# Kernel tuning notes

Hardware: AMD Instinct MI355X
Metric: run time of the kernel (lower is better)

## Reference

```python
import jax, jax.numpy as jnp
import numpy as np

B, S, D_MODEL, D_ATTN = 4, 2048, 1024, 1024
NEG_INF = jnp.float32(-jnp.inf)


def setup_inputs() -> dict:
    key = jax.random.key(0)
    ks = jax.random.split(key, 6)
    scale = 1.0 / np.sqrt(D_MODEL)
    return {
        "x": jax.random.normal(ks[0], (B, S, D_MODEL), dtype=jnp.float32),
        "mask": jnp.ones((B, S), dtype=jnp.float32),
        "Wq": jax.random.normal(ks[1], (D_ATTN, D_MODEL), dtype=jnp.float32) * scale,
        "Wk": jax.random.normal(ks[2], (D_ATTN, D_MODEL), dtype=jnp.float32) * scale,
        "Wv": jax.random.normal(ks[3], (D_ATTN, D_MODEL), dtype=jnp.float32) * scale,
        "Wo": jax.random.normal(ks[4], (D_MODEL, D_ATTN), dtype=jnp.float32) * scale,
        "bo": jnp.zeros((D_MODEL,), dtype=jnp.float32),
    }


def reference(x, mask, Wq, Wk, Wv, Wo, bo):
    # x: [B,S,Dm]; torch Linear weight is [out,in], so y = x @ W.T
    q = jnp.einsum("bsd,ad->bsa", x, Wq)  # [B,S,Da]
    k = jnp.einsum("bsd,ad->bsa", x, Wk)
    v = jnp.einsum("bsd,ad->bsa", x, Wv)  # NOTE: v from x (original quirk)
    logits = jnp.einsum("bqa,bka->bqk", q, k)  # [B,S,S]
    # causal mask (cross_attention=True path): keep lower triangle incl. diag
    causal = jnp.tril(jnp.ones((S, S), dtype=bool))
    logits = jnp.where(causal[None], logits, NEG_INF)
    # padding mask: outer product of per-token mask
    square_mask = mask[:, :, None] * mask[:, None, :]  # [B,S,S]
    logits = jnp.where(square_mask == 1, logits, NEG_INF)
    # scale by sqrt(d_model) AFTER masking (as in original)
    attn = jax.nn.softmax(logits / jnp.sqrt(jnp.float32(D_MODEL)), axis=-1)
    attn_out = jnp.einsum("bqk,bka->bqa", attn, v)  # [B,S,Da]
    return jnp.einsum("bsa,da->bsd", attn_out, Wo) + bo
```

## Files before the change

kernel.cpp:

```cpp
#include <hip/hip_runtime.h>
#include <hip/hip_bf16.h>
#include <cstdio>

typedef __bf16 bf16x8 __attribute__((ext_vector_type(8)));
typedef float f32x4 __attribute__((ext_vector_type(4)));

#define BM 128
#define BN 128
#define BK 64

__device__ __forceinline__ unsigned short f2bf(float f) {
  union { float f; unsigned u; } v; v.f = f;
  unsigned u = v.u;
  return (unsigned short)((u + 0x7FFFu + ((u >> 16) & 1u)) >> 16);
}

__device__ __forceinline__ float bf2f(unsigned short s) {
  union { unsigned u; float f; } v; v.u = ((unsigned)s) << 16;
  return v.f;
}

#define GLOAD16(gsrc, ldst) \
  __builtin_amdgcn_global_load_lds((const __attribute__((address_space(1))) void*)(gsrc), \
                                   (__attribute__((address_space(3))) void*)(ldst), 16, 0, 0)

template<int EPI>
__global__ __launch_bounds__(256, 2)
void gemm_bt(const unsigned short* __restrict__ A, const unsigned short* __restrict__ B,
             void* __restrict__ Cv, void* __restrict__ Cv2, const float* __restrict__ bias,
             int K, int ldA, int ldB, int ldC,
             long aBat, long bBat, long cBat,
             int causalSkip, int causalKlim, float scale, int revM)
{
  const int gx = gridDim.x;
  const int nwg = gx * gridDim.y;
  const int flat = blockIdx.y * gx + blockIdx.x;
  const int qch = nwg >> 3, rch = nwg & 7;
  const int xcd = flat & 7, idx = flat >> 3;
  const int swz = (xcd < rch ? xcd * (qch + 1) : rch * (qch + 1) + (xcd - rch) * qch) + idx;
  const int bx = swz % gx;
  int by = swz / gx;
  if (revM) by = gridDim.y - 1 - by;

  const int m0 = by * BM;
  const int n0 = bx * BN;
  if (causalSkip && n0 > m0) return;
  const int bz = blockIdx.z;

  const unsigned short* Ab = A + (long)bz * aBat + (long)m0 * ldA;
  const unsigned short* Bb = B + (long)bz * bBat + (long)n0 * ldB;

  __shared__ short lds[2][2][BM * BK];

  const int tid = threadIdx.x;
  const int lane = tid & 63;
  const int wave = tid >> 6;
  const int wr = wave >> 1, wc = wave & 1;

  const int Keff = causalKlim ? min(K, m0 + BM) : K;
  const int nk = Keff / BK;

  const int srow = tid >> 3;
  const int sch = tid & 7;

  const f32x4 fzero = {0.f, 0.f, 0.f, 0.f};
  f32x4 acc[4][4];
#pragma unroll
  for (int i = 0; i < 4; i++)
#pragma unroll
    for (int j = 0; j < 4; j++) acc[i][j] = fzero;

  int aOff[4][2], bOff[4][2];
#pragma unroll
  for (int i = 0; i < 4; i++) {
#pragma unroll
    for (int s = 0; s < 2; s++) {
      int ra = wr * 64 + i * 16 + (lane & 15);
      aOff[i][s] = ra * BK + (((s * 4 + (lane >> 4)) ^ (ra & 7)) * 8);
      int rb = wc * 64 + i * 16 + (lane & 15);
      bOff[i][s] = rb * BK + (((s * 4 + (lane >> 4)) ^ (rb & 7)) * 8);
    }
  }

  auto stage = [&](int buf, int kt) {
    const unsigned short* Ak = Ab + kt * BK;
    const unsigned short* Bk = Bb + kt * BK;
#pragma unroll
    for (int r = 0; r < 4; r++) {
      int row = r * 32 + srow;
      int sc = sch ^ (row & 7);
      GLOAD16(Ak + (long)row * ldA + sc * 8, &lds[buf][0][(r * 32 + wave * 8) * BK]);
    }
#pragma unroll
    for (int r = 0; r < 4; r++) {
      int row = r * 32 + srow;
      int sc = sch ^ (row & 7);
      GLOAD16(Bk + (long)row * ldB + sc * 8, &lds[buf][1][(r * 32 + wave * 8) * BK]);
    }
  };

  stage(0, 0);
  stage(1, 1);
  asm volatile("s_waitcnt vmcnt(8)" ::: "memory");
  __builtin_amdgcn_sched_barrier(0);
  __builtin_amdgcn_s_barrier();

  int cur = 0;
  for (int kt = 0; kt < nk; kt++) {
    const short* La = lds[cur][0];
    const short* Lb = lds[cur][1];
    bf16x8 av[2][4], bv[2][4];
#pragma unroll
    for (int s = 0; s < 2; s++) {
#pragma unroll
      for (int i = 0; i < 4; i++) {
        av[s][i] = *reinterpret_cast<const bf16x8*>(La + aOff[i][s]);
        bv[s][i] = *reinterpret_cast<const bf16x8*>(Lb + bOff[i][s]);
      }
    }
    asm volatile("s_waitcnt lgkmcnt(0)" ::: "memory");
    __builtin_amdgcn_sched_barrier(0);
    __builtin_amdgcn_s_barrier();
    __builtin_amdgcn_sched_barrier(0);

    if (kt + 2 < nk) {
      stage(cur, kt + 2);
      asm volatile("s_waitcnt vmcnt(8)" ::: "memory");
    } else if (kt + 1 < nk) {
      asm volatile("s_waitcnt vmcnt(0)" ::: "memory");
    }
    if (kt + 1 < nk) {
      __builtin_amdgcn_s_barrier();
      __builtin_amdgcn_sched_barrier(0);
    }

    __builtin_amdgcn_s_setprio(1);
#pragma unroll
    for (int s = 0; s < 2; s++)
#pragma unroll
      for (int i = 0; i < 4; i++)
#pragma unroll
        for (int j = 0; j < 4; j++)
          acc[i][j] = __builtin_amdgcn_mfma_f32_16x16x32_bf16(av[s][i], bv[s][j], acc[i][j], 0, 0, 0);
    __builtin_amdgcn_s_setprio(0);
    __builtin_amdgcn_sched_barrier(0);
    cur ^= 1;
  }

  const int rb4 = (lane >> 4) * 4;
  const int cl = lane & 15;
#pragma unroll
  for (int i = 0; i < 4; i++) {
#pragma unroll
    for (int j = 0; j < 4; j++) {
      const int gm = m0 + wr * 64 + i * 16 + rb4;
      const int gn = n0 + wc * 64 + j * 16 + cl;
      if (EPI == 0) {
        unsigned short* C = (unsigned short*)Cv + (long)bz * cBat;
#pragma unroll
        for (int r = 0; r < 4; r++)
          C[(long)(gm + r) * ldC + gn] = f2bf(acc[i][j][r] * scale);
      } else if (EPI == 2) {
        float* C = (float*)Cv;
        const float bb = bias[gn];
#pragma unroll
        for (int r = 0; r < 4; r++)
          C[(long)(gm + r) * ldC + gn] = acc[i][j][r] + bb;
      } else if (EPI == 4) {
        if (gn < 2048) {
          unsigned short* C = (unsigned short*)Cv;
#pragma unroll
          for (int r = 0; r < 4; r++)
            C[(long)(gm + r) * ldC + gn] = f2bf(acc[i][j][r]);
        } else {
          const int d = gn - 2048;
          const int b = gm >> 11;
          const int sIdx = gm & 2047;
          unsigned short* C = (unsigned short*)Cv2 + (long)b * (2048L * 1024)
                              + (long)d * 2048 + sIdx;
          ushort4 pk;
          pk.x = f2bf(acc[i][j][0]);
          pk.y = f2bf(acc[i][j][1]);
          pk.z = f2bf(acc[i][j][2]);
          pk.w = f2bf(acc[i][j][3]);
          *reinterpret_cast<ushort4*>(C) = pk;
        }
      }
    }
  }
}

__global__ __launch_bounds__(256)
void softmax_rows(const unsigned short* __restrict__ Sb, const float* __restrict__ maskv,
                  unsigned short* __restrict__ P, int Sdim)
{
  const int q = blockIdx.x;
  const int b = blockIdx.y;
  const int kmax = (q & ~127) + 128;
  const unsigned short* row = Sb + ((long)b * Sdim + q) * Sdim;
  unsigned short* prow = P + ((long)b * Sdim + q) * Sdim;
  const float* mrow = maskv + (long)b * Sdim;
  const int tid = threadIdx.x;
  const float mq = mrow[q];
  const int k0 = tid * 8;
  const bool live = (k0 < kmax);

  float v[8];
  if (live) {
    uint4 raw = *reinterpret_cast<const uint4*>(row + k0);
    const unsigned short* us = reinterpret_cast<const unsigned short*>(&raw);
    float4 ma = *reinterpret_cast<const float4*>(mrow + k0);
    float4 mb = *reinterpret_cast<const float4*>(mrow + k0 + 4);
    float mv[8] = {ma.x, ma.y, ma.z, ma.w, mb.x, mb.y, mb.z, mb.w};
#pragma unroll
    for (int u = 0; u < 8; u++) {
      const int k = k0 + u;
      const bool ok = (k <= q) && (mq * mv[u] == 1.0f);
      v[u] = ok ? bf2f(us[u]) : -INFINITY;
    }
  } else {
#pragma unroll
    for (int u = 0; u < 8; u++) v[u] = -INFINITY;
  }

  float mx = -INFINITY;
#pragma unroll
  for (int u = 0; u < 8; u++) mx = fmaxf(mx, v[u]);
#pragma unroll
  for (int o = 32; o; o >>= 1) mx = fmaxf(mx, __shfl_xor(mx, o));
  __shared__ float redm[4], reds[4];
  if ((tid & 63) == 0) redm[tid >> 6] = mx;
  __syncthreads();
  mx = fmaxf(fmaxf(redm[0], redm[1]), fmaxf(redm[2], redm[3]));

  float p[8];
  float sm = 0.f;
#pragma unroll
  for (int u = 0; u < 8; u++) {
    p[u] = (v[u] > -INFINITY) ? __expf(v[u] - mx) : 0.f;
    sm += p[u];
  }
#pragma unroll
  for (int o = 32; o; o >>= 1) sm += __shfl_xor(sm, o);
  if ((tid & 63) == 0) reds[tid >> 6] = sm;
  __syncthreads();
  sm = reds[0] + reds[1] + reds[2] + reds[3];
  const float inv = 1.0f / sm;

  if (live) {
    union { unsigned short us[8]; uint4 u4; } pk;
#pragma unroll
    for (int u = 0; u < 8; u++) pk.us[u] = f2bf(p[u] * inv);
    *reinterpret_cast<uint4*>(prow + k0) = pk.u4;
  }
}

__global__ __launch_bounds__(256)
void cast_f32_bf16(const float* __restrict__ in, unsigned short* __restrict__ out, int n)
{
  const int i = (blockIdx.x * 256 + threadIdx.x) * 8;
  if (i >= n) return;
  float4 a = *reinterpret_cast<const float4*>(in + i);
  float4 b = *reinterpret_cast<const float4*>(in + i + 4);
  union { unsigned short us[8]; uint4 u4; } pk;
  pk.us[0] = f2bf(a.x); pk.us[1] = f2bf(a.y); pk.us[2] = f2bf(a.z); pk.us[3] = f2bf(a.w);
  pk.us[4] = f2bf(b.x); pk.us[5] = f2bf(b.y); pk.us[6] = f2bf(b.z); pk.us[7] = f2bf(b.w);
  *reinterpret_cast<uint4*>(out + i) = pk.u4;
}

__global__ __launch_bounds__(256)
void cast_weights(const float* __restrict__ w0, const float* __restrict__ w1,
                  const float* __restrict__ w2, const float* __restrict__ w3,
                  unsigned short* __restrict__ dqkv, unsigned short* __restrict__ dout)
{
  const int z = blockIdx.z;
  const float* src = (z == 0) ? w0 : (z == 1) ? w1 : (z == 2) ? w2 : w3;
  unsigned short* dst = (z < 3) ? (dqkv + (long)z * 1024 * 1024) : dout;
  const int i = (blockIdx.x * 256 + threadIdx.x) * 8;
  float4 a = *reinterpret_cast<const float4*>(src + i);
  float4 b = *reinterpret_cast<const float4*>(src + i + 4);
  union { unsigned short us[8]; uint4 u4; } pk;
  pk.us[0] = f2bf(a.x); pk.us[1] = f2bf(a.y); pk.us[2] = f2bf(a.z); pk.us[3] = f2bf(a.w);
  pk.us[4] = f2bf(b.x); pk.us[5] = f2bf(b.y); pk.us[6] = f2bf(b.z); pk.us[7] = f2bf(b.w);
  *reinterpret_cast<uint4*>(dst + i) = pk.u4;
}

extern "C" void kernel_launch(void* const* d_in, const int* in_sizes, int n_in,
                              void* d_out, int out_size, void* d_ws, size_t ws_size,
                              hipStream_t stream)
{
  const int B = 4, S = 2048, D = 1024;
  const float* x  = (const float*)d_in[0];
  const float* mk = (const float*)d_in[1];
  const float* Wq = (const float*)d_in[2];
  const float* Wk = (const float*)d_in[3];
  const float* Wv = (const float*)d_in[4];
  const float* Wo = (const float*)d_in[5];
  const float* bo = (const float*)d_in[6];
  float* out = (float*)d_out;

  char* ws = (char*)d_ws;
  const long MB = 1024L * 1024L;
  unsigned short* Xbf  = (unsigned short*)(ws + 0);
  unsigned short* QKb  = (unsigned short*)(ws + 16 * MB);
  unsigned short* Vt   = (unsigned short*)(ws + 48 * MB);
  unsigned short* Wqkv = (unsigned short*)(ws + 64 * MB);
  unsigned short* Wob  = (unsigned short*)(ws + 70 * MB);
  unsigned short* Sbuf = (unsigned short*)(ws + 72 * MB);
  unsigned short* P    = QKb;
  unsigned short* O    = Xbf;

  if (ws_size < (size_t)(104 * MB)) {
    fprintf(stderr, "kernel_launch: ws too small (%zu bytes, need 104MB)\n", ws_size);
    return;
  }

  cast_f32_bf16<<<dim3((B * S * D) / 8 / 256), 256, 0, stream>>>(x, Xbf, B * S * D);
  cast_weights<<<dim3((D * D) / 8 / 256, 1, 4), 256, 0, stream>>>(Wq, Wk, Wv, Wo, Wqkv, Wob);

  const dim3 blk(256);
  dim3 gQKV(3072 / BN, 8192 / BM, 1);
  gemm_bt<4><<<gQKV, blk, 0, stream>>>(Xbf, Wqkv, QKb, Vt, nullptr,
                                       1024, 1024, 1024, 2048,
                                       0, 0, 0, 0, 0, 1.0f, 0);
  dim3 gS(2048 / BN, 2048 / BM, 4);
  gemm_bt<0><<<gS, blk, 0, stream>>>(QKb, QKb + 1024, Sbuf, nullptr, nullptr,
                                     1024, 2048, 2048, 2048,
                                     (long)S * 2048, (long)S * 2048, (long)S * S,
                                     1, 0, 0.03125f, 0);
  softmax_rows<<<dim3(2048, 4), blk, 0, stream>>>(Sbuf, mk, P, 2048);
  dim3 gO(1024 / BN, 2048 / BM, 4);
  gemm_bt<0><<<gO, blk, 0, stream>>>(P, Vt, O, nullptr, nullptr,
                                     2048, 2048, 2048, 1024,
                                     (long)S * S, (long)D * S, (long)S * D,
                                     0, 1, 1.0f, 1);
  dim3 gF(1024 / BN, 8192 / BM, 1);
  gemm_bt<2><<<gF, blk, 0, stream>>>(O, Wob, out, nullptr, bo,
                                     1024, 1024, 1024, 1024,
                                     0, 0, 0, 0, 0, 1.0f, 0);
}
```

Baseline: 180.7 us.

## Widen GEMM tile to 128x256 with 8 waves and interleaved quarter-step pipeline

GEMM blocks grow to 512 threads (8 waves in a 2x4 layout) covering 128x256 output tiles. Each k-step is split into four MFMA quarters interleaved with LDS fragment loads and staggered global-to-LDS staging of the next A and B tiles. The causal skip test is adjusted to the wider N tile. The two cast kernels are merged into a single launch. The aim is more operand reuse per LDS byte and better overlap of memory with MFMA, at the cost of one block per CU, fewer blocks for the smaller GEMMs, and more wasted work in causal tiles.

```diff
diff --git a/kernel.cpp b/kernel.cpp
--- a/kernel.cpp
+++ b/kernel.cpp
@@ -6,7 +6,7 @@
 typedef float f32x4 __attribute__((ext_vector_type(4)));
 
 #define BM 128
-#define BN 128
+#define BN 256
 #define BK 64
 
 __device__ __forceinline__ unsigned short f2bf(float f) {
@@ -25,7 +25,7 @@
                                    (__attribute__((address_space(3))) void*)(ldst), 16, 0, 0)
 
 template<int EPI>
-__global__ __launch_bounds__(256, 2)
+__global__ __launch_bounds__(512, 1)
 void gemm_bt(const unsigned short* __restrict__ A, const unsigned short* __restrict__ B,
              void* __restrict__ Cv, void* __restrict__ Cv2, const float* __restrict__ bias,
              int K, int ldA, int ldB, int ldC,
@@ -44,18 +44,19 @@
 
   const int m0 = by * BM;
   const int n0 = bx * BN;
-  if (causalSkip && n0 > m0) return;
+  if (causalSkip && n0 > m0 + (BM - 1)) return;
   const int bz = blockIdx.z;
 
   const unsigned short* Ab = A + (long)bz * aBat + (long)m0 * ldA;
   const unsigned short* Bb = B + (long)bz * bBat + (long)n0 * ldB;
 
-  __shared__ short lds[2][2][BM * BK];
+  __shared__ short ldsA[2][BM * BK];
+  __shared__ short ldsB[2][BN * BK];
 
   const int tid = threadIdx.x;
   const int lane = tid & 63;
   const int wave = tid >> 6;
-  const int wr = wave >> 1, wc = wave & 1;
+  const int wr = wave >> 2, wc = wave & 3;
 
   const int Keff = causalKlim ? min(K, m0 + BM) : K;
   const int nk = Keff / BK;
@@ -72,79 +73,133 @@
 
   int aOff[4][2], bOff[4][2];
 #pragma unroll
-  for (int i = 0; i < 4; i++) {
-#pragma unroll
-    for (int s = 0; s < 2; s++) {
-      int ra = wr * 64 + i * 16 + (lane & 15);
-      aOff[i][s] = ra * BK + (((s * 4 + (lane >> 4)) ^ (ra & 7)) * 8);
-      int rb = wc * 64 + i * 16 + (lane & 15);
-      bOff[i][s] = rb * BK + (((s * 4 + (lane >> 4)) ^ (rb & 7)) * 8);
-    }
-  }
-
-  auto stage = [&](int buf, int kt) {
+  for (int f = 0; f < 4; f++) {
+#pragma unroll
+    for (int k = 0; k < 2; k++) {
+      int ra = wr * 64 + f * 16 + (lane & 15);
+      aOff[f][k] = ra * BK + (((k * 4 + (lane >> 4)) ^ (ra & 7)) * 8);
+      int rb = wc * 64 + f * 16 + (lane & 15);
+      bOff[f][k] = rb * BK + (((k * 4 + (lane >> 4)) ^ (rb & 7)) * 8);
+    }
+  }
+
+  auto stageA = [&](int buf, int kt) {
     const unsigned short* Ak = Ab + kt * BK;
+#pragma unroll
+    for (int L = 0; L < 2; L++) {
+      int row = L * 64 + srow;
+      int sc = sch ^ (row & 7);
+      GLOAD16(Ak + (long)row * ldA + sc * 8, &ldsA[buf][row * BK + sch * 8]);
+    }
+  };
+  auto stageB = [&](int buf, int kt, int h) {
     const unsigned short* Bk = Bb + kt * BK;
 #pragma unroll
-    for (int r = 0; r < 4; r++) {
-      int row = r * 32 + srow;
+    for (int L = 0; L < 2; L++) {
+      int row = h * 128 + L * 64 + srow;
       int sc = sch ^ (row & 7);
-      GLOAD16(Ak + (long)row * ldA + sc * 8, &lds[buf][0][(r * 32 + wave * 8) * BK]);
-    }
-#pragma unroll
-    for (int r = 0; r < 4; r++) {
-      int row = r * 32 + srow;
-      int sc = sch ^ (row & 7);
-      GLOAD16(Bk + (long)row * ldB + sc * 8, &lds[buf][1][(r * 32 + wave * 8) * BK]);
+      GLOAD16(Bk + (long)row * ldB + sc * 8, &ldsB[buf][row * BK + sch * 8]);
     }
   };
 
-  stage(0, 0);
-  stage(1, 1);
-  asm volatile("s_waitcnt vmcnt(8)" ::: "memory");
+  stageA(0, 0); stageB(0, 0, 0); stageB(0, 0, 1);
+  if (nk > 1) {
+    stageB(1, 1, 0); stageB(1, 1, 1);
+    asm volatile("s_waitcnt vmcnt(4)" ::: "memory");
+  } else {
+    asm volatile("s_waitcnt vmcnt(0)" ::: "memory");
+  }
   __builtin_amdgcn_sched_barrier(0);
   __builtin_amdgcn_s_barrier();
-
-  int cur = 0;
+  __builtin_amdgcn_sched_barrier(0);
+
   for (int kt = 0; kt < nk; kt++) {
-    const short* La = lds[cur][0];
-    const short* Lb = lds[cur][1];
-    bf16x8 av[2][4], bv[2][4];
-#pragma unroll
-    for (int s = 0; s < 2; s++) {
-#pragma unroll
-      for (int i = 0; i < 4; i++) {
-        av[s][i] = *reinterpret_cast<const bf16x8*>(La + aOff[i][s]);
-        bv[s][i] = *reinterpret_cast<const bf16x8*>(Lb + bOff[i][s]);
-      }
-    }
+    const int cur = kt & 1;
+    const short* La = ldsA[cur];
+    const short* Lb = ldsB[cur];
+    bf16x8 a01[2][2], a23[2][2], b01[2][2], b23[2][2];
+
+#pragma unroll
+    for (int m = 0; m < 2; m++)
+#pragma unroll
+      for (int k = 0; k < 2; k++) a01[m][k] = *reinterpret_cast<const bf16x8*>(La + aOff[m][k]);
+#pragma unroll
+    for (int n = 0; n < 2; n++)
+#pragma unroll
+      for (int k = 0; k < 2; k++) b01[n][k] = *reinterpret_cast<const bf16x8*>(Lb + bOff[n][k]);
+    if (kt + 1 < nk) stageA(cur ^ 1, kt + 1);
+    __builtin_amdgcn_s_barrier();
     asm volatile("s_waitcnt lgkmcnt(0)" ::: "memory");
     __builtin_amdgcn_sched_barrier(0);
-    __builtin_amdgcn_s_barrier();
+    __builtin_amdgcn_s_setprio(1);
+#pragma unroll
+    for (int m = 0; m < 2; m++)
+#pragma unroll
+      for (int n = 0; n < 2; n++)
+#pragma unroll
+        for (int k = 0; k < 2; k++)
+          acc[m][n] = __builtin_amdgcn_mfma_f32_16x16x32_bf16(a01[m][k], b01[n][k], acc[m][n], 0, 0, 0);
+    __builtin_amdgcn_s_setprio(0);
+    __builtin_amdgcn_s_barrier();
+
+#pragma unroll
+    for (int n = 0; n < 2; n++)
+#pragma unroll
+      for (int k = 0; k < 2; k++) b23[n][k] = *reinterpret_cast<const bf16x8*>(Lb + bOff[n + 2][k]);
+    __builtin_amdgcn_s_barrier();
+    asm volatile("s_waitcnt lgkmcnt(0)" ::: "memory");
     __builtin_amdgcn_sched_barrier(0);
-
-    if (kt + 2 < nk) {
-      stage(cur, kt + 2);
-      asm volatile("s_waitcnt vmcnt(8)" ::: "memory");
-    } else if (kt + 1 < nk) {
-      asm volatile("s_waitcnt vmcnt(0)" ::: "memory");
-    }
+    __builtin_amdgcn_s_setprio(1);
+#pragma unroll
+    for (int m = 0; m < 2; m++)
+#pragma unroll
+      for (int n = 0; n < 2; n++)
+#pragma unroll
+        for (int k = 0; k < 2; k++)
+          acc[m][n + 2] = __builtin_amdgcn_mfma_f32_16x16x32_bf16(a01[m][k], b23[n][k], acc[m][n + 2], 0, 0, 0);
+    __builtin_amdgcn_s_setprio(0);
+    __builtin_amdgcn_s_barrier();
+
+#pragma unroll
+    for (int m = 0; m < 2; m++)
+#pragma unroll
+      for (int k = 0; k < 2; k++) a23[m][k] = *reinterpret_cast<const bf16x8*>(La + aOff[m + 2][k]);
+    if (kt + 2 < nk) stageB(cur, kt + 2, 0);
+    __builtin_amdgcn_s_barrier();
+    asm volatile("s_waitcnt lgkmcnt(0)" ::: "memory");
+    __builtin_amdgcn_sched_barrier(0);
+    __builtin_amdgcn_s_setprio(1);
+#pragma unroll
+    for (int m = 0; m < 2; m++)
+#pragma unroll
+      for (int n = 0; n < 2; n++)
+#pragma unroll
+        for (int k = 0; k < 2; k++)
+          acc[m + 2][n] = __builtin_amdgcn_mfma_f32_16x16x32_bf16(a23[m][k], b01[n][k], acc[m + 2][n], 0, 0, 0);
+    __builtin_amdgcn_s_setprio(0);
+    __builtin_amdgcn_s_barrier();
+
+    if (kt + 2 < nk) stageB(cur, kt + 2, 1);
+    __builtin_amdgcn_s_barrier();
+    __builtin_amdgcn_s_setprio(1);
+#pragma unroll
+    for (int m = 0; m < 2; m++)
+#pragma unroll
+      for (int n = 0; n < 2; n++)
+#pragma unroll
+        for (int k = 0; k < 2; k++)
+          acc[m + 2][n + 2] = __builtin_amdgcn_mfma_f32_16x16x32_bf16(a23[m][k], b23[n][k], acc[m + 2][n + 2], 0, 0, 0);
+    __builtin_amdgcn_s_setprio(0);
     if (kt + 1 < nk) {
+      if (kt + 2 < nk) {
+        asm volatile("s_waitcnt vmcnt(4)" ::: "memory");
+      } else {
+        asm volatile("s_waitcnt vmcnt(0)" ::: "memory");
+      }
+      __builtin_amdgcn_sched_barrier(0);
       __builtin_amdgcn_s_barrier();
       __builtin_amdgcn_sched_barrier(0);
     }
-
-    __builtin_amdgcn_s_setprio(1);
-#pragma unroll
-    for (int s = 0; s < 2; s++)
-#pragma unroll
-      for (int i = 0; i < 4; i++)
-#pragma unroll
-        for (int j = 0; j < 4; j++)
-          acc[i][j] = __builtin_amdgcn_mfma_f32_16x16x32_bf16(av[s][i], bv[s][j], acc[i][j], 0, 0, 0);
-    __builtin_amdgcn_s_setprio(0);
-    __builtin_amdgcn_sched_barrier(0);
-    cur ^= 1;
   }
 
   const int rb4 = (lane >> 4) * 4;
@@ -256,27 +311,25 @@
 }
 
 __global__ __launch_bounds__(256)
-void cast_f32_bf16(const float* __restrict__ in, unsigned short* __restrict__ out, int n)
+void cast_all(const float* __restrict__ x, const float* __restrict__ w0,
+              const float* __restrict__ w1, const float* __restrict__ w2,
+              const float* __restrict__ w3,
+              unsigned short* __restrict__ xb, unsigned short* __restrict__ dqkv,
+              unsigned short* __restrict__ dout)
 {
-  const int i = (blockIdx.x * 256 + threadIdx.x) * 8;
-  if (i >= n) return;
-  float4 a = *reinterpret_cast<const float4*>(in + i);
-  float4 b = *reinterpret_cast<const float4*>(in + i + 4);
-  union { unsigned short us[8]; uint4 u4; } pk;
-  pk.us[0] = f2bf(a.x); pk.us[1] = f2bf(a.y); pk.us[2] = f2bf(a.z); pk.us[3] = f2bf(a.w);
-  pk.us[4] = f2bf(b.x); pk.us[5] = f2bf(b.y); pk.us[6] = f2bf(b.z); pk.us[7] = f2bf(b.w);
-  *reinterpret_cast<uint4*>(out + i) = pk.u4;
-}
-
-__global__ __launch_bounds__(256)
-void cast_weights(const float* __restrict__ w0, const float* __restrict__ w1,
-                  const float* __restrict__ w2, const float* __restrict__ w3,
-                  unsigned short* __restrict__ dqkv, unsigned short* __restrict__ dout)
-{
-  const int z = blockIdx.z;
-  const float* src = (z == 0) ? w0 : (z == 1) ? w1 : (z == 2) ? w2 : w3;
-  unsigned short* dst = (z < 3) ? (dqkv + (long)z * 1024 * 1024) : dout;
-  const int i = (blockIdx.x * 256 + threadIdx.x) * 8;
+  const int blk = blockIdx.x;
+  const float* src;
+  unsigned short* dst;
+  int i;
+  if (blk < 4096) {
+    src = x; dst = xb; i = (blk * 256 + threadIdx.x) * 8;
+  } else {
+    const int w = (blk - 4096) >> 9;
+    const int off = (blk - 4096) & 511;
+    src = (w == 0) ? w0 : (w == 1) ? w1 : (w == 2) ? w2 : w3;
+    dst = (w < 3) ? (dqkv + (long)w * 1024 * 1024) : dout;
+    i = (off * 256 + threadIdx.x) * 8;
+  }
   float4 a = *reinterpret_cast<const float4*>(src + i);
   float4 b = *reinterpret_cast<const float4*>(src + i + 4);
   union { unsigned short us[8]; uint4 u4; } pk;
@@ -315,10 +368,9 @@
     return;
   }
 
-  cast_f32_bf16<<<dim3((B * S * D) / 8 / 256), 256, 0, stream>>>(x, Xbf, B * S * D);
-  cast_weights<<<dim3((D * D) / 8 / 256, 1, 4), 256, 0, stream>>>(Wq, Wk, Wv, Wo, Wqkv, Wob);
-
-  const dim3 blk(256);
+  cast_all<<<dim3(4096 + 2048), 256, 0, stream>>>(x, Wq, Wk, Wv, Wo, Xbf, Wqkv, Wob);
+
+  const dim3 blk(512);
   dim3 gQKV(3072 / BN, 8192 / BM, 1);
   gemm_bt<4><<<gQKV, blk, 0, stream>>>(Xbf, Wqkv, QKb, Vt, nullptr,
                                        1024, 1024, 1024, 2048,
@@ -328,7 +380,7 @@
                                      1024, 2048, 2048, 2048,
                                      (long)S * 2048, (long)S * 2048, (long)S * S,
                                      1, 0, 0.03125f, 0);
-  softmax_rows<<<dim3(2048, 4), blk, 0, stream>>>(Sbuf, mk, P, 2048);
+  softmax_rows<<<dim3(2048, 4), dim3(256), 0, stream>>>(Sbuf, mk, P, 2048);
   dim3 gO(1024 / BN, 2048 / BM, 4);
   gemm_bt<0><<<gO, blk, 0, stream>>>(P, Vt, O, nullptr, nullptr,
                                      2048, 2048, 2048, 1024,
```

New measurement: 214.9 us. 18.9% more time.

## Add 256x256-tile 8-wave GEMM for QKV projection and merge cast kernels

Applied to the files above, without the earlier changes.

Replaces the 128x128 QKV projection GEMM with a dedicated 256x256-tile kernel using 512 threads, double-buffered LDS staged by direct global-to-LDS loads, and a staggered A/B prefetch interleaved with four MFMA phases. The larger tile raises arithmetic intensity and cuts global traffic for the biggest GEMM. In exchange it uses one block per CU and a 384-block grid, which may leave CUs underfilled. The x and weight cast kernels are also merged into one launch to save launch overhead.

```diff
diff --git a/kernel.cpp b/kernel.cpp
--- a/kernel.cpp
+++ b/kernel.cpp
@@ -24,10 +24,203 @@
   __builtin_amdgcn_global_load_lds((const __attribute__((address_space(1))) void*)(gsrc), \
                                    (__attribute__((address_space(3))) void*)(ldst), 16, 0, 0)
 
+__global__ __launch_bounds__(512, 1)
+void gemm256_qkv(const unsigned short* __restrict__ A, const unsigned short* __restrict__ B,
+                 unsigned short* __restrict__ QK, unsigned short* __restrict__ Vt,
+                 int K, int ldA, int ldB)
+{
+  const int gx = gridDim.x;
+  const int nwg = gx * gridDim.y;
+  const int flat = blockIdx.y * gx + blockIdx.x;
+  const int qch = nwg >> 3, rch = nwg & 7;
+  const int xcd = flat & 7, idx = flat >> 3;
+  const int swz = (xcd < rch ? xcd * (qch + 1) : rch * (qch + 1) + (xcd - rch) * qch) + idx;
+  const int bx = swz % gx;
+  const int by = swz / gx;
+  const int m0 = by * 256, n0 = bx * 256;
+
+  const unsigned short* Ab = A + (long)m0 * ldA;
+  const unsigned short* Bb = B + (long)n0 * ldB;
+
+  __shared__ short ldsA[2][2][128 * 64];
+  __shared__ short ldsB[2][2][128 * 64];
+
+  const int tid = threadIdx.x;
+  const int lane = tid & 63;
+  const int wave = tid >> 6;
+  const int wr = wave >> 2, wc = wave & 3;
+
+  const int nk = K / 64;
+
+  const int srow = tid >> 3;
+  const int sch = tid & 7;
+  const int ssc = sch ^ (srow & 7);
+
+  f32x4 acc[8][4];
+  const f32x4 fzero = {0.f, 0.f, 0.f, 0.f};
+#pragma unroll
+  for (int i = 0; i < 8; i++)
+#pragma unroll
+    for (int j = 0; j < 4; j++) acc[i][j] = fzero;
+
+  const int rowbase = (lane & 15) * 64;
+  const int x0 = (((lane >> 4) + 0) ^ (lane & 7)) * 8;
+  const int x1 = (((lane >> 4) + 4) ^ (lane & 7)) * 8;
+
+  auto stageA = [&](int buf, int kt, int h) {
+    const unsigned short* src = Ab + (long)(h * 128) * ldA + kt * 64;
+#pragma unroll
+    for (int L = 0; L < 2; L++) {
+      int row = L * 64 + srow;
+      GLOAD16(src + (long)row * ldA + ssc * 8, &ldsA[buf][h][row * 64 + sch * 8]);
+    }
+  };
+  auto stageB = [&](int buf, int kt, int h) {
+    const unsigned short* src = Bb + (long)(h * 128) * ldB + kt * 64;
+#pragma unroll
+    for (int L = 0; L < 2; L++) {
+      int row = L * 64 + srow;
+      GLOAD16(src + (long)row * ldB + ssc * 8, &ldsB[buf][h][row * 64 + sch * 8]);
+    }
+  };
+
+  stageA(0, 0, 0); stageA(0, 0, 1); stageB(0, 0, 0); stageB(0, 0, 1);
+  if (nk > 1) {
+    stageB(1, 1, 0); stageB(1, 1, 1);
+    asm volatile("s_waitcnt vmcnt(4)" ::: "memory");
+  } else {
+    asm volatile("s_waitcnt vmcnt(0)" ::: "memory");
+  }
+  __builtin_amdgcn_sched_barrier(0);
+  __builtin_amdgcn_s_barrier();
+  __builtin_amdgcn_sched_barrier(0);
+
+  for (int kt = 0; kt < nk; kt++) {
+    const int c = kt & 1;
+    const short* pa = &ldsA[c][wr][rowbase];
+    const short* pb = &ldsB[c][wc >> 1][(wc & 1) * 4096 + rowbase];
+    bf16x8 b[4][2];
+    bf16x8 a[2][2];
+
+#pragma unroll
+    for (int f = 0; f < 2; f++) {
+      a[f][0] = *reinterpret_cast<const bf16x8*>(pa + f * 1024 + x0);
+      a[f][1] = *reinterpret_cast<const bf16x8*>(pa + f * 1024 + x1);
+    }
+#pragma unroll
+    for (int f = 0; f < 4; f++) {
+      b[f][0] = *reinterpret_cast<const bf16x8*>(pb + f * 1024 + x0);
+      b[f][1] = *reinterpret_cast<const bf16x8*>(pb + f * 1024 + x1);
+    }
+    if (kt + 1 < nk) { stageA(c ^ 1, kt + 1, 0); stageA(c ^ 1, kt + 1, 1); }
+    asm volatile("s_waitcnt lgkmcnt(0)" ::: "memory");
+    __builtin_amdgcn_sched_barrier(0);
+    __builtin_amdgcn_s_setprio(1);
+#pragma unroll
+    for (int f = 0; f < 2; f++)
+#pragma unroll
+      for (int j = 0; j < 4; j++)
+#pragma unroll
+        for (int k = 0; k < 2; k++)
+          acc[f][j] = __builtin_amdgcn_mfma_f32_16x16x32_bf16(a[f][k], b[j][k], acc[f][j], 0, 0, 0);
+    __builtin_amdgcn_s_setprio(0);
+    __builtin_amdgcn_s_barrier();
+
+#pragma unroll
+    for (int f = 0; f < 2; f++) {
+      a[f][0] = *reinterpret_cast<const bf16x8*>(pa + (f + 2) * 1024 + x0);
+      a[f][1] = *reinterpret_cast<const bf16x8*>(pa + (f + 2) * 1024 + x1);
+    }
+    if (kt + 2 < nk) stageB(c, kt + 2, 0);
+    asm volatile("s_waitcnt lgkmcnt(0)" ::: "memory");
+    __builtin_amdgcn_sched_barrier(0);
+    __builtin_amdgcn_s_setprio(1);
+#pragma unroll
+    for (int f = 0; f < 2; f++)
+#pragma unroll
+      for (int j = 0; j < 4; j++)
+#pragma unroll
+        for (int k = 0; k < 2; k++)
+          acc[f + 2][j] = __builtin_amdgcn_mfma_f32_16x16x32_bf16(a[f][k], b[j][k], acc[f + 2][j], 0, 0, 0);
+    __builtin_amdgcn_s_setprio(0);
+    __builtin_amdgcn_s_barrier();
+
+#pragma unroll
+    for (int f = 0; f < 2; f++) {
+      a[f][0] = *reinterpret_cast<const bf16x8*>(pa + (f + 4) * 1024 + x0);
+      a[f][1] = *reinterpret_cast<const bf16x8*>(pa + (f + 4) * 1024 + x1);
+    }
+    if (kt + 2 < nk) stageB(c, kt + 2, 1);
+    asm volatile("s_waitcnt lgkmcnt(0)" ::: "memory");
+    __builtin_amdgcn_sched_barrier(0);
+    __builtin_amdgcn_s_setprio(1);
+#pragma unroll
+    for (int f = 0; f < 2; f++)
+#pragma unroll
+      for (int j = 0; j < 4; j++)
+#pragma unroll
+        for (int k = 0; k < 2; k++)
+          acc[f + 4][j] = __builtin_amdgcn_mfma_f32_16x16x32_bf16(a[f][k], b[j][k], acc[f + 4][j], 0, 0, 0);
+    __builtin_amdgcn_s_setprio(0);
+    __builtin_amdgcn_s_barrier();
+
+#pragma unroll
+    for (int f = 0; f < 2; f++) {
+      a[f][0] = *reinterpret_cast<const bf16x8*>(pa + (f + 6) * 1024 + x0);
+      a[f][1] = *reinterpret_cast<const bf16x8*>(pa + (f + 6) * 1024 + x1);
+    }
+    asm volatile("s_waitcnt lgkmcnt(0)" ::: "memory");
+    __builtin_amdgcn_sched_barrier(0);
+    __builtin_amdgcn_s_setprio(1);
+#pragma unroll
+    for (int f = 0; f < 2; f++)
+#pragma unroll
+      for (int j = 0; j < 4; j++)
+#pragma unroll
+        for (int k = 0; k < 2; k++)
+          acc[f + 6][j] = __builtin_amdgcn_mfma_f32_16x16x32_bf16(a[f][k], b[j][k], acc[f + 6][j], 0, 0, 0);
+    __builtin_amdgcn_s_setprio(0);
+    if (kt + 1 < nk) {
+      if (kt + 2 < nk) asm volatile("s_waitcnt vmcnt(4)" ::: "memory");
+      else             asm volatile("s_waitcnt vmcnt(0)" ::: "memory");
+      __builtin_amdgcn_sched_barrier(0);
+    }
+    __builtin_amdgcn_s_barrier();
+    __builtin_amdgcn_sched_barrier(0);
+  }
+
+  const int rb4 = (lane >> 4) * 4;
+  const int cl = lane & 15;
+#pragma unroll
+  for (int fi = 0; fi < 8; fi++) {
+#pragma unroll
+    for (int fj = 0; fj < 4; fj++) {
+      const int gm = m0 + wr * 128 + fi * 16 + rb4;
+      const int gn = n0 + wc * 64 + fj * 16 + cl;
+      if (gn < 2048) {
+#pragma unroll
+        for (int r = 0; r < 4; r++)
+          QK[(long)(gm + r) * 2048 + gn] = f2bf(acc[fi][fj][r]);
+      } else {
+        const int d = gn - 2048;
+        const int bb = gm >> 11;
+        const int sIdx = gm & 2047;
+        unsigned short* C = Vt + (long)bb * (2048L * 1024) + (long)d * 2048 + sIdx;
+        ushort4 pk;
+        pk.x = f2bf(acc[fi][fj][0]);
+        pk.y = f2bf(acc[fi][fj][1]);
+        pk.z = f2bf(acc[fi][fj][2]);
+        pk.w = f2bf(acc[fi][fj][3]);
+        *reinterpret_cast<ushort4*>(C) = pk;
+      }
+    }
+  }
+}
+
 template<int EPI>
 __global__ __launch_bounds__(256, 2)
 void gemm_bt(const unsigned short* __restrict__ A, const unsigned short* __restrict__ B,
-             void* __restrict__ Cv, void* __restrict__ Cv2, const float* __restrict__ bias,
+             void* __restrict__ Cv, const float* __restrict__ bias,
              int K, int ldA, int ldB, int ldC,
              long aBat, long bBat, long cBat,
              int causalSkip, int causalKlim, float scale, int revM)
@@ -160,31 +353,12 @@
 #pragma unroll
         for (int r = 0; r < 4; r++)
           C[(long)(gm + r) * ldC + gn] = f2bf(acc[i][j][r] * scale);
-      } else if (EPI == 2) {
+      } else {
         float* C = (float*)Cv;
         const float bb = bias[gn];
 #pragma unroll
         for (int r = 0; r < 4; r++)
           C[(long)(gm + r) * ldC + gn] = acc[i][j][r] + bb;
-      } else if (EPI == 4) {
-        if (gn < 2048) {
-          unsigned short* C = (unsigned short*)Cv;
-#pragma unroll
-          for (int r = 0; r < 4; r++)
-            C[(long)(gm + r) * ldC + gn] = f2bf(acc[i][j][r]);
-        } else {
-          const int d = gn - 2048;
-          const int b = gm >> 11;
-          const int sIdx = gm & 2047;
-          unsigned short* C = (unsigned short*)Cv2 + (long)b * (2048L * 1024)
-                              + (long)d * 2048 + sIdx;
-          ushort4 pk;
-          pk.x = f2bf(acc[i][j][0]);
-          pk.y = f2bf(acc[i][j][1]);
-          pk.z = f2bf(acc[i][j][2]);
-          pk.w = f2bf(acc[i][j][3]);
-          *reinterpret_cast<ushort4*>(C) = pk;
-        }
       }
     }
   }
@@ -256,27 +430,25 @@
 }
 
 __global__ __launch_bounds__(256)
-void cast_f32_bf16(const float* __restrict__ in, unsigned short* __restrict__ out, int n)
+void cast_all(const float* __restrict__ x, const float* __restrict__ w0,
+              const float* __restrict__ w1, const float* __restrict__ w2,
+              const float* __restrict__ w3,
+              unsigned short* __restrict__ xb, unsigned short* __restrict__ dqkv,
+              unsigned short* __restrict__ dout)
 {
-  const int i = (blockIdx.x * 256 + threadIdx.x) * 8;
-  if (i >= n) return;
-  float4 a = *reinterpret_cast<const float4*>(in + i);
-  float4 b = *reinterpret_cast<const float4*>(in + i + 4);
-  union { unsigned short us[8]; uint4 u4; } pk;
-  pk.us[0] = f2bf(a.x); pk.us[1] = f2bf(a.y); pk.us[2] = f2bf(a.z); pk.us[3] = f2bf(a.w);
-  pk.us[4] = f2bf(b.x); pk.us[5] = f2bf(b.y); pk.us[6] = f2bf(b.z); pk.us[7] = f2bf(b.w);
-  *reinterpret_cast<uint4*>(out + i) = pk.u4;
-}
-
-__global__ __launch_bounds__(256)
-void cast_weights(const float* __restrict__ w0, const float* __restrict__ w1,
-                  const float* __restrict__ w2, const float* __restrict__ w3,
-                  unsigned short* __restrict__ dqkv, unsigned short* __restrict__ dout)
-{
-  const int z = blockIdx.z;
-  const float* src = (z == 0) ? w0 : (z == 1) ? w1 : (z == 2) ? w2 : w3;
-  unsigned short* dst = (z < 3) ? (dqkv + (long)z * 1024 * 1024) : dout;
-  const int i = (blockIdx.x * 256 + threadIdx.x) * 8;
+  const int blk = blockIdx.x;
+  const float* src;
+  unsigned short* dst;
+  int i;
+  if (blk < 4096) {
+    src = x; dst = xb; i = (blk * 256 + threadIdx.x) * 8;
+  } else {
+    const int w = (blk - 4096) >> 9;
+    const int off = (blk - 4096) & 511;
+    src = (w == 0) ? w0 : (w == 1) ? w1 : (w == 2) ? w2 : w3;
+    dst = (w < 3) ? (dqkv + (long)w * 1024 * 1024) : dout;
+    i = (off * 256 + threadIdx.x) * 8;
+  }
   float4 a = *reinterpret_cast<const float4*>(src + i);
   float4 b = *reinterpret_cast<const float4*>(src + i + 4);
   union { unsigned short us[8]; uint4 u4; } pk;
@@ -315,27 +487,24 @@
     return;
   }
 
-  cast_f32_bf16<<<dim3((B * S * D) / 8 / 256), 256, 0, stream>>>(x, Xbf, B * S * D);
-  cast_weights<<<dim3((D * D) / 8 / 256, 1, 4), 256, 0, stream>>>(Wq, Wk, Wv, Wo, Wqkv, Wob);
+  cast_all<<<dim3(4096 + 2048), 256, 0, stream>>>(x, Wq, Wk, Wv, Wo, Xbf, Wqkv, Wob);
+
+  gemm256_qkv<<<dim3(12, 32), dim3(512), 0, stream>>>(Xbf, Wqkv, QKb, Vt, 1024, 1024, 1024);
 
   const dim3 blk(256);
-  dim3 gQKV(3072 / BN, 8192 / BM, 1);
-  gemm_bt<4><<<gQKV, blk, 0, stream>>>(Xbf, Wqkv, QKb, Vt, nullptr,
-                                       1024, 1024, 1024, 2048,
-                                       0, 0, 0, 0, 0, 1.0f, 0);
   dim3 gS(2048 / BN, 2048 / BM, 4);
-  gemm_bt<0><<<gS, blk, 0, stream>>>(QKb, QKb + 1024, Sbuf, nullptr, nullptr,
+  gemm_bt<0><<<gS, blk, 0, stream>>>(QKb, QKb + 1024, Sbuf, nullptr,
                                      1024, 2048, 2048, 2048,
                                      (long)S * 2048, (long)S * 2048, (long)S * S,
                                      1, 0, 0.03125f, 0);
   softmax_rows<<<dim3(2048, 4), blk, 0, stream>>>(Sbuf, mk, P, 2048);
   dim3 gO(1024 / BN, 2048 / BM, 4);
-  gemm_bt<0><<<gO, blk, 0, stream>>>(P, Vt, O, nullptr, nullptr,
+  gemm_bt<0><<<gO, blk, 0, stream>>>(P, Vt, O, nullptr,
                                      2048, 2048, 2048, 1024,
                                      (long)S * S, (long)D * S, (long)S * D,
                                      0, 1, 1.0f, 1);
   dim3 gF(1024 / BN, 8192 / BM, 1);
-  gemm_bt<2><<<gF, blk, 0, stream>>>(O, Wob, out, nullptr, bo,
+  gemm_bt<2><<<gF, blk, 0, stream>>>(O, Wob, out, bo,
                                      1024, 1024, 1024, 1024,
                                      0, 0, 0, 0, 0, 1.0f, 0);
 }
```

Measured after the change: 189.7 us. +5.0%, slower.
